# Optimization experiments

Measured on AMD Instinct MI355X. Metric: run time of the kernel, lower is better.

The kernel has to match this reference:

```python
import jax, jax.numpy as jnp
import numpy as np

B, T, D, H = 4, 4096, 1280, 5120  # batch, tokens (64x64 SAM grid), embedding_dim, mlp_dim


def setup_inputs() -> dict:
    key = jax.random.key(0)
    k = jax.random.split(key, 5)
    # int8 quantized activations and weights (symmetric, per-tensor)
    x = jax.random.randint(k[0], (B, T, D), -128, 128, dtype=jnp.int8)
    w1 = jax.random.randint(k[1], (H, D), -128, 128, dtype=jnp.int8)  # lin1.weight [out,in]
    b1 = jax.random.normal(k[2], (H,), jnp.float32) * 0.02            # fp32 bias
    w2 = jax.random.randint(k[3], (D, H), -128, 128, dtype=jnp.int8)  # lin2.weight [out,in]
    b2 = jax.random.normal(k[4], (D,), jnp.float32) * 0.02
    a1 = jnp.float32(0.05 * 0.01)   # input_scale * w1_scale (dequant alpha of lin1)
    s_req = jnp.float32(0.08)       # lin2_input_scale (requant scale after GELU)
    a2 = jnp.float32(0.08 * 0.01)   # lin2_input_scale * w2_scale (dequant alpha of lin2)
    return dict(x=x, w1=w1, b1=b1, w2=w2, b2=b2, a1=a1, s_req=s_req, a2=a2)


def reference(x, w1, b1, w2, b2, a1, s_req, a2):
    acc1 = jnp.einsum('btd,hd->bth', x.astype(jnp.int32), w1.astype(jnp.int32))
    h = acc1.astype(jnp.float32) * a1 + b1              # [B,T,H] fp32
    # exact (erf) GELU, then requantize to int8 for lin2's input
    g = jax.nn.gelu(h, approximate=False)
    q = jnp.clip(jnp.round(g / s_req), -128, 127).astype(jnp.int8)
    acc2 = jnp.einsum('bth,dh->btd', q.astype(jnp.int32), w2.astype(jnp.int32))
    return acc2.astype(jnp.float32) * a2 + b2           # [B,T,D] fp32
```

## Files before the change

kernel.cpp:

```cpp
#include <hip/hip_runtime.h>
#include <stdint.h>
#include <math.h>

typedef __attribute__((ext_vector_type(4))) int i32x4;
typedef __attribute__((ext_vector_type(16))) int i32x16;
typedef __attribute__((ext_vector_type(4))) float f32x4;

constexpr int D_DIM = 1280;
constexpr int H_DIM = 5120;

__device__ __forceinline__ void gload_lds16(const void* g, void* l) {
  __builtin_amdgcn_global_load_lds(
      (const __attribute__((address_space(1))) void*)g,
      (__attribute__((address_space(3))) void*)l,
      16, 0, 0);
}

__global__ void __launch_bounds__(256) k_packw(const int* __restrict__ s1,
                                               const int* __restrict__ s2,
                                               int8_t* __restrict__ out,
                                               long wn) {
  long i = ((long)blockIdx.x * 256 + threadIdx.x) * 16;
  const int* p = (i < wn) ? (s1 + i) : (s2 + (i - wn));
  i32x4 a = *(const i32x4*)(p);
  i32x4 b = *(const i32x4*)(p + 4);
  i32x4 c = *(const i32x4*)(p + 8);
  i32x4 d = *(const i32x4*)(p + 12);
  i32x4 r;
  r.x = (a.x & 255) | ((a.y & 255) << 8) | ((a.z & 255) << 16) | (a.w << 24);
  r.y = (b.x & 255) | ((b.y & 255) << 8) | ((b.z & 255) << 16) | (b.w << 24);
  r.z = (c.x & 255) | ((c.y & 255) << 8) | ((c.z & 255) << 16) | (c.w << 24);
  r.w = (d.x & 255) | ((d.y & 255) << 8) | ((d.z & 255) << 16) | (d.w << 24);
  *(i32x4*)(out + i) = r;
}

__global__ void __launch_bounds__(256) k_pack(const int* __restrict__ in,
                                              int8_t* __restrict__ out,
                                              long n) {
  long i = ((long)blockIdx.x * 256 + threadIdx.x) * 16;
  if (i >= n) return;
  const int* p = in + i;
  i32x4 a = *(const i32x4*)(p);
  i32x4 b = *(const i32x4*)(p + 4);
  i32x4 c = *(const i32x4*)(p + 8);
  i32x4 d = *(const i32x4*)(p + 12);
  i32x4 r;
  r.x = (a.x & 255) | ((a.y & 255) << 8) | ((a.z & 255) << 16) | (a.w << 24);
  r.y = (b.x & 255) | ((b.y & 255) << 8) | ((b.z & 255) << 16) | (b.w << 24);
  r.z = (c.x & 255) | ((c.y & 255) << 8) | ((c.z & 255) << 16) | (c.w << 24);
  r.w = (d.x & 255) | ((d.y & 255) << 8) | ((d.z & 255) << 16) | (d.w << 24);
  *(i32x4*)(out + i) = r;
}

template <int KDIM, int NDIM, bool GELU>
__global__ void __launch_bounds__(256, 2)
k_gemm(const int8_t* __restrict__ A, const int8_t* __restrict__ B,
       const float* __restrict__ bias, const float* __restrict__ ps1,
       const float* __restrict__ ps2, void* __restrict__ Cout, int Mtiles) {
  constexpr int BM = 128, BN = 128, BKB = 128;
  constexpr int NT = KDIM / BKB;
  constexpr int BNC = NDIM / BN;
  constexpr int G = BNC * 4;

  __shared__ __align__(16) int8_t smem[4 * 16384];

  const int nwg = Mtiles * BNC;
  int bm, bn;
  {
    const int bid = blockIdx.x;
    const int q = nwg >> 3, r = nwg & 7, x = bid & 7, l = bid >> 3;
    const int swz = (x < r ? x * (q + 1) : r * (q + 1) + (x - r) * q) + l;
    if ((Mtiles & 3) == 0) {
      const int g = swz / G, rr = swz % G;
      bn = rr >> 2;
      bm = g * 4 + (rr & 3);
    } else {
      bn = swz % BNC;
      bm = swz / BNC;
    }
  }

  const int tid = threadIdx.x;
  const int lane = tid & 63, wid = tid >> 6;
  const int wr = wid >> 1, wc = wid & 1;

  const int srow = tid >> 3;
  const int soff = (((tid & 7) ^ (srow & 7)) << 4);
  const int8_t* Ath = A + (size_t)(bm * BM + srow) * KDIM + soff;
  const int8_t* Bth = B + (size_t)(bn * BN + srow) * KDIM + soff;
  const int dT = tid * 16;

  auto STAGE = [&](int boff, const int8_t* ga, const int8_t* gb) {
#pragma unroll
    for (int p = 0; p < 4; ++p)
      gload_lds16(ga + (size_t)(p * 32) * KDIM, smem + boff + dT + p * 4096);
#pragma unroll
    for (int p = 0; p < 4; ++p)
      gload_lds16(gb + (size_t)(p * 32) * KDIM,
                  smem + 32768 + boff + dT + p * 4096);
  };

  const int r32 = lane & 31, hi5 = lane >> 5;
  const int fsw = (lane & 7) << 4;
  const int kq = hi5 << 4;
  const int8_t* aP[4];
  const int8_t* bP[4];
#pragma unroll
  for (int ks = 0; ks < 4; ++ks) {
    const int koff = (ks * 32 + kq) ^ fsw;
    aP[ks] = smem + (wr * 64 + r32) * BKB + koff;
    bP[ks] = smem + 32768 + (wc * 64 + r32) * BKB + koff;
  }

  i32x16 acc[2][2] = {};

  auto COMPUTE = [&](int boff) {
#pragma unroll
    for (int ks = 0; ks < 4; ++ks) {
      i32x4 a0 = *(const i32x4*)(aP[ks] + boff);
      i32x4 a1 = *(const i32x4*)(aP[ks] + boff + 4096);
      i32x4 b0 = *(const i32x4*)(bP[ks] + boff);
      i32x4 b1 = *(const i32x4*)(bP[ks] + boff + 4096);
      if constexpr (GELU) {
        acc[0][0] = __builtin_amdgcn_mfma_i32_32x32x32_i8(b0, a0, acc[0][0], 0, 0, 0);
        acc[0][1] = __builtin_amdgcn_mfma_i32_32x32x32_i8(b0, a1, acc[0][1], 0, 0, 0);
        acc[1][0] = __builtin_amdgcn_mfma_i32_32x32x32_i8(b1, a0, acc[1][0], 0, 0, 0);
        acc[1][1] = __builtin_amdgcn_mfma_i32_32x32x32_i8(b1, a1, acc[1][1], 0, 0, 0);
      } else {
        acc[0][0] = __builtin_amdgcn_mfma_i32_32x32x32_i8(a0, b0, acc[0][0], 0, 0, 0);
        acc[0][1] = __builtin_amdgcn_mfma_i32_32x32x32_i8(a0, b1, acc[0][1], 0, 0, 0);
        acc[1][0] = __builtin_amdgcn_mfma_i32_32x32x32_i8(a1, b0, acc[1][0], 0, 0, 0);
        acc[1][1] = __builtin_amdgcn_mfma_i32_32x32x32_i8(a1, b1, acc[1][1], 0, 0, 0);
      }
    }
  };

  STAGE(0, Ath, Bth);
  __syncthreads();
  const int8_t* gA = Ath + BKB;
  const int8_t* gB = Bth + BKB;
#pragma unroll 1
  for (int t = 0; t < NT; t += 2) {
    STAGE(16384, gA, gB);
    COMPUTE(0);
    __syncthreads();
    if (t + 2 < NT) STAGE(0, gA + BKB, gB + BKB);
    COMPUTE(16384);
    __syncthreads();
    gA += 2 * BKB;
    gB += 2 * BKB;
  }

  if constexpr (GELU) {
    const float s1 = *ps1;
    const float rs = 1.0f / (*ps2);
    int8_t* Q = (int8_t*)Cout;
    int8_t* lb = smem;
#pragma unroll
    for (int n = 0; n < 2; ++n) {
#pragma unroll
      for (int q = 0; q < 4; ++q) {
        const int hl = wc * 64 + n * 32 + q * 8 + hi5 * 4;
        const f32x4 bv = *(const f32x4*)(bias + bn * BN + hl);
#pragma unroll
        for (int m = 0; m < 2; ++m) {
          const int tok = wr * 64 + m * 32 + r32;
          uint32_t pk = 0;
#pragma unroll
          for (int rr = 0; rr < 4; ++rr) {
            const float h = __builtin_fmaf((float)acc[n][m][q * 4 + rr], s1, bv[rr]);
            const float e = __expf(-1.702f * h);
            const float g = h * __builtin_amdgcn_rcpf(1.0f + e);
            float qf = rintf(g * rs);
            qf = fminf(127.0f, fmaxf(-128.0f, qf));
            pk |= ((uint32_t)((int)qf & 255)) << (rr * 8);
          }
          *(uint32_t*)(lb + tok * 132 + hl) = pk;
        }
      }
    }
    __syncthreads();
#pragma unroll
    for (int it = 0; it < 4; ++it) {
      const int row = it * 32 + (tid >> 3);
      const int sl = tid & 7;
      const int8_t* rp = lb + row * 132 + sl * 16;
      i32x4 v;
      v.x = *(const int*)(rp);
      v.y = *(const int*)(rp + 4);
      v.z = *(const int*)(rp + 8);
      v.w = *(const int*)(rp + 12);
      *(i32x4*)(Q + (size_t)(bm * BM + row) * NDIM + bn * BN + sl * 16) = v;
    }
  } else {
    const float s1 = *ps1;
    float* O = (float*)Cout;
    const int colb = bn * BN + wc * 64 + r32;
#pragma unroll
    for (int n = 0; n < 2; ++n) {
      const int col = colb + n * 32;
      const float bv = bias[col];
#pragma unroll
      for (int m = 0; m < 2; ++m) {
        const int rowb = bm * BM + wr * 64 + m * 32 + hi5 * 4;
#pragma unroll
        for (int q = 0; q < 4; ++q)
#pragma unroll
          for (int rr = 0; rr < 4; ++rr) {
            const int row = rowb + q * 8 + rr;
            O[(size_t)row * NDIM + col] =
                __builtin_fmaf((float)acc[m][n][q * 4 + rr], s1, bv);
          }
      }
    }
  }
}

extern "C" void kernel_launch(void* const* d_in, const int* in_sizes, int n_in,
                              void* d_out, int out_size, void* d_ws, size_t ws_size,
                              hipStream_t stream) {
  (void)in_sizes; (void)n_in; (void)out_size;
  const int*   x32  = (const int*)d_in[0];
  const int*   w132 = (const int*)d_in[1];
  const float* b1   = (const float*)d_in[2];
  const int*   w232 = (const int*)d_in[3];
  const float* b2   = (const float*)d_in[4];
  const float* a1   = (const float*)d_in[5];
  const float* sreq = (const float*)d_in[6];
  const float* a2   = (const float*)d_in[7];
  float* out = (float*)d_out;

  const int M = 4 * 4096;
  const size_t WN = (size_t)H_DIM * D_DIM;
  constexpr int BM = 128, BN = 128;

  int8_t* w1p  = (int8_t*)d_ws;
  int8_t* w2p  = w1p + WN;
  int8_t* base = w2p + WN;

  size_t avail = ws_size > 2 * WN ? ws_size - 2 * WN : 0;
  size_t rows = avail / (size_t)(D_DIM + H_DIM);
  int Mc = (int)((rows / BM) * BM);
  if (Mc > M) Mc = M;
  if (Mc < BM) Mc = BM;

  k_packw<<<(int)(2 * WN / 4096), 256, 0, stream>>>(w132, w232, w1p, (long)WN);

  for (int m0 = 0; m0 < M; m0 += Mc) {
    const int mc = (M - m0 < Mc) ? (M - m0) : Mc;
    int8_t* xp = base;
    int8_t* q  = base + (size_t)Mc * D_DIM;
    const size_t nx = (size_t)mc * D_DIM;
    const int mt = mc / BM;
    k_pack<<<(int)(nx / 4096), 256, 0, stream>>>(x32 + (size_t)m0 * D_DIM, xp, (long)nx);
    k_gemm<D_DIM, H_DIM, true><<<mt * (H_DIM / BN), 256, 0, stream>>>(
        xp, w1p, b1, a1, sreq, q, mt);
    k_gemm<H_DIM, D_DIM, false><<<mt * (D_DIM / BN), 256, 0, stream>>>(
        q, w2p, b2, a2, nullptr, out + (size_t)m0 * D_DIM, mt);
  }
}
```

Baseline: 284.4 us.

## Triple-buffer A tiles with asynchronous vmcnt waits and MFMA priority hints

Reworks the GEMM main loop from a two-stage double buffer with full __syncthreads into a pipeline: the A tile uses three LDS slots, B uses two, and loads are issued one or two iterations ahead. Explicit s_waitcnt vmcnt plus a raw s_barrier replace the per-half syncthreads, and s_setprio raises wave priority around the MFMA bursts. The goal is to hide global-to-LDS latency and reduce barrier stalls. LDS use grows from 64KB to 80KB per block, which may limit two blocks per CU, and the hand-set vmcnt counts must match the number of loads in flight.

```diff
diff --git a/kernel.cpp b/kernel.cpp
--- a/kernel.cpp
+++ b/kernel.cpp
@@ -61,8 +61,9 @@
   constexpr int NT = KDIM / BKB;
   constexpr int BNC = NDIM / BN;
   constexpr int G = BNC * 4;
-
-  __shared__ __align__(16) int8_t smem[4 * 16384];
+  constexpr int BOFF = 49152;
+
+  __shared__ __align__(16) int8_t smem[81920];
 
   const int nwg = Mtiles * BNC;
   int bm, bn;
@@ -90,37 +91,41 @@
   const int8_t* Bth = B + (size_t)(bn * BN + srow) * KDIM + soff;
   const int dT = tid * 16;
 
-  auto STAGE = [&](int boff, const int8_t* ga, const int8_t* gb) {
+  auto STAGE_A = [&](int slot, int tt) {
+    const int8_t* g = Ath + tt * BKB;
 #pragma unroll
     for (int p = 0; p < 4; ++p)
-      gload_lds16(ga + (size_t)(p * 32) * KDIM, smem + boff + dT + p * 4096);
+      gload_lds16(g + (size_t)(p * 32) * KDIM, smem + slot * 16384 + dT + p * 4096);
+  };
+  auto STAGE_B = [&](int slot, int tt) {
+    const int8_t* g = Bth + tt * BKB;
 #pragma unroll
     for (int p = 0; p < 4; ++p)
-      gload_lds16(gb + (size_t)(p * 32) * KDIM,
-                  smem + 32768 + boff + dT + p * 4096);
+      gload_lds16(g + (size_t)(p * 32) * KDIM,
+                  smem + BOFF + slot * 16384 + dT + p * 4096);
   };
 
   const int r32 = lane & 31, hi5 = lane >> 5;
   const int fsw = (lane & 7) << 4;
   const int kq = hi5 << 4;
-  const int8_t* aP[4];
-  const int8_t* bP[4];
-#pragma unroll
-  for (int ks = 0; ks < 4; ++ks) {
-    const int koff = (ks * 32 + kq) ^ fsw;
-    aP[ks] = smem + (wr * 64 + r32) * BKB + koff;
-    bP[ks] = smem + 32768 + (wc * 64 + r32) * BKB + koff;
-  }
+  int koff[4];
+#pragma unroll
+  for (int ks = 0; ks < 4; ++ks) koff[ks] = ((ks * 32 + kq) ^ fsw);
+  const int rowA = (wr * 64 + r32) * BKB;
+  const int rowB = (wc * 64 + r32) * BKB;
 
   i32x16 acc[2][2] = {};
 
-  auto COMPUTE = [&](int boff) {
+  auto COMPUTE = [&](int aoff, int boff) {
+    const int8_t* Ab = smem + aoff + rowA;
+    const int8_t* Bb = smem + BOFF + boff + rowB;
 #pragma unroll
     for (int ks = 0; ks < 4; ++ks) {
-      i32x4 a0 = *(const i32x4*)(aP[ks] + boff);
-      i32x4 a1 = *(const i32x4*)(aP[ks] + boff + 4096);
-      i32x4 b0 = *(const i32x4*)(bP[ks] + boff);
-      i32x4 b1 = *(const i32x4*)(bP[ks] + boff + 4096);
+      i32x4 a0 = *(const i32x4*)(Ab + koff[ks]);
+      i32x4 a1 = *(const i32x4*)(Ab + 4096 + koff[ks]);
+      i32x4 b0 = *(const i32x4*)(Bb + koff[ks]);
+      i32x4 b1 = *(const i32x4*)(Bb + 4096 + koff[ks]);
+      __builtin_amdgcn_s_setprio(1);
       if constexpr (GELU) {
         acc[0][0] = __builtin_amdgcn_mfma_i32_32x32x32_i8(b0, a0, acc[0][0], 0, 0, 0);
         acc[0][1] = __builtin_amdgcn_mfma_i32_32x32x32_i8(b0, a1, acc[0][1], 0, 0, 0);
@@ -132,26 +137,33 @@
         acc[1][0] = __builtin_amdgcn_mfma_i32_32x32x32_i8(a1, b0, acc[1][0], 0, 0, 0);
         acc[1][1] = __builtin_amdgcn_mfma_i32_32x32x32_i8(a1, b1, acc[1][1], 0, 0, 0);
       }
+      __builtin_amdgcn_s_setprio(0);
     }
   };
 
-  STAGE(0, Ath, Bth);
-  __syncthreads();
-  const int8_t* gA = Ath + BKB;
-  const int8_t* gB = Bth + BKB;
+  STAGE_B(0, 0);
+  STAGE_A(0, 0);
+  STAGE_A(1, 1);
+
+  int acur = 0;
+  int astg = 2;
 #pragma unroll 1
-  for (int t = 0; t < NT; t += 2) {
-    STAGE(16384, gA, gB);
-    COMPUTE(0);
+  for (int t = 0; t < NT; ++t) {
+    if (t + 1 < NT)
+      asm volatile("s_waitcnt vmcnt(4)" ::: "memory");
+    else
+      asm volatile("s_waitcnt vmcnt(0)" ::: "memory");
+    __builtin_amdgcn_s_barrier();
+    __builtin_amdgcn_sched_barrier(0);
+    if (t + 1 < NT) STAGE_B((t + 1) & 1, t + 1);
+    if (t + 2 < NT) STAGE_A(astg, t + 2);
+    COMPUTE(acur * 16384, (t & 1) * 16384);
+    acur = acur == 2 ? 0 : acur + 1;
+    astg = astg == 2 ? 0 : astg + 1;
+  }
+
+  if constexpr (GELU) {
     __syncthreads();
-    if (t + 2 < NT) STAGE(0, gA + BKB, gB + BKB);
-    COMPUTE(16384);
-    __syncthreads();
-    gA += 2 * BKB;
-    gB += 2 * BKB;
-  }
-
-  if constexpr (GELU) {
     const float s1 = *ps1;
     const float rs = 1.0f / (*ps2);
     int8_t* Q = (int8_t*)Cout;
```

Result: slower. 302.3 us (+6.3%).

## Load weight fragments directly into registers instead of staging through LDS

Applied to the files above, without the earlier changes.

The weight operand is no longer copied into shared memory. Each wave reads its MFMA weight fragments straight from global memory into registers, double-buffered one K-step ahead, so shared memory holds only the activation tile (32 KB instead of 64 KB). This removes half of the LDS traffic and LDS reads per step, and raises MFMA issue priority with s_setprio around each MFMA group. In exchange, the two waves sharing a column block each fetch the same weights, the global reads are strided per row rather than staged cooperatively, and register pressure goes up.

```diff
diff --git a/kernel.cpp b/kernel.cpp
--- a/kernel.cpp
+++ b/kernel.cpp
@@ -54,7 +54,7 @@
 
 template <int KDIM, int NDIM, bool GELU>
 __global__ void __launch_bounds__(256, 2)
-k_gemm(const int8_t* __restrict__ A, const int8_t* __restrict__ B,
+k_gemm(const int8_t* __restrict__ A, const int8_t* __restrict__ W,
        const float* __restrict__ bias, const float* __restrict__ ps1,
        const float* __restrict__ ps2, void* __restrict__ Cout, int Mtiles) {
   constexpr int BM = 128, BN = 128, BKB = 128;
@@ -62,7 +62,7 @@
   constexpr int BNC = NDIM / BN;
   constexpr int G = BNC * 4;
 
-  __shared__ __align__(16) int8_t smem[4 * 16384];
+  __shared__ __align__(16) int8_t smem[32768];
 
   const int nwg = Mtiles * BNC;
   int bm, bn;
@@ -83,72 +83,75 @@
   const int tid = threadIdx.x;
   const int lane = tid & 63, wid = tid >> 6;
   const int wr = wid >> 1, wc = wid & 1;
+  const int r32 = lane & 31, hi5 = lane >> 5;
 
   const int srow = tid >> 3;
   const int soff = (((tid & 7) ^ (srow & 7)) << 4);
   const int8_t* Ath = A + (size_t)(bm * BM + srow) * KDIM + soff;
-  const int8_t* Bth = B + (size_t)(bn * BN + srow) * KDIM + soff;
   const int dT = tid * 16;
 
-  auto STAGE = [&](int boff, const int8_t* ga, const int8_t* gb) {
+  auto STAGE = [&](int boff, int tt) {
+    const int8_t* g = Ath + tt * BKB;
 #pragma unroll
     for (int p = 0; p < 4; ++p)
-      gload_lds16(ga + (size_t)(p * 32) * KDIM, smem + boff + dT + p * 4096);
-#pragma unroll
-    for (int p = 0; p < 4; ++p)
-      gload_lds16(gb + (size_t)(p * 32) * KDIM,
-                  smem + 32768 + boff + dT + p * 4096);
+      gload_lds16(g + (size_t)(p * 32) * KDIM, smem + boff + dT + p * 4096);
   };
 
-  const int r32 = lane & 31, hi5 = lane >> 5;
+  const int8_t* W0 = W + (size_t)(bn * BN + wc * 64 + r32) * KDIM + (hi5 << 4);
+  const int8_t* W1p = W0 + (size_t)32 * KDIM;
+  i32x4 wfA[8], wfB[8];
+  auto LOADW = [&](i32x4 (&wf)[8], int tt) {
+    const int o = tt * BKB;
+#pragma unroll
+    for (int ks = 0; ks < 4; ++ks) {
+      wf[2 * ks]     = *(const i32x4*)(W0 + o + ks * 32);
+      wf[2 * ks + 1] = *(const i32x4*)(W1p + o + ks * 32);
+    }
+  };
+
   const int fsw = (lane & 7) << 4;
   const int kq = hi5 << 4;
-  const int8_t* aP[4];
-  const int8_t* bP[4];
-#pragma unroll
-  for (int ks = 0; ks < 4; ++ks) {
-    const int koff = (ks * 32 + kq) ^ fsw;
-    aP[ks] = smem + (wr * 64 + r32) * BKB + koff;
-    bP[ks] = smem + 32768 + (wc * 64 + r32) * BKB + koff;
-  }
+  int koff[4];
+#pragma unroll
+  for (int ks = 0; ks < 4; ++ks) koff[ks] = ((ks * 32 + kq) ^ fsw);
+  const int rowA = (wr * 64 + r32) * BKB;
 
   i32x16 acc[2][2] = {};
 
-  auto COMPUTE = [&](int boff) {
+  auto COMPUTE = [&](int boff, const i32x4 (&wf)[8]) {
+    const int8_t* Ab = smem + boff + rowA;
 #pragma unroll
     for (int ks = 0; ks < 4; ++ks) {
-      i32x4 a0 = *(const i32x4*)(aP[ks] + boff);
-      i32x4 a1 = *(const i32x4*)(aP[ks] + boff + 4096);
-      i32x4 b0 = *(const i32x4*)(bP[ks] + boff);
-      i32x4 b1 = *(const i32x4*)(bP[ks] + boff + 4096);
+      i32x4 a0 = *(const i32x4*)(Ab + koff[ks]);
+      i32x4 a1 = *(const i32x4*)(Ab + 4096 + koff[ks]);
+      __builtin_amdgcn_s_setprio(1);
       if constexpr (GELU) {
-        acc[0][0] = __builtin_amdgcn_mfma_i32_32x32x32_i8(b0, a0, acc[0][0], 0, 0, 0);
-        acc[0][1] = __builtin_amdgcn_mfma_i32_32x32x32_i8(b0, a1, acc[0][1], 0, 0, 0);
-        acc[1][0] = __builtin_amdgcn_mfma_i32_32x32x32_i8(b1, a0, acc[1][0], 0, 0, 0);
-        acc[1][1] = __builtin_amdgcn_mfma_i32_32x32x32_i8(b1, a1, acc[1][1], 0, 0, 0);
+        acc[0][0] = __builtin_amdgcn_mfma_i32_32x32x32_i8(wf[2*ks],   a0, acc[0][0], 0, 0, 0);
+        acc[0][1] = __builtin_amdgcn_mfma_i32_32x32x32_i8(wf[2*ks],   a1, acc[0][1], 0, 0, 0);
+        acc[1][0] = __builtin_amdgcn_mfma_i32_32x32x32_i8(wf[2*ks+1], a0, acc[1][0], 0, 0, 0);
+        acc[1][1] = __builtin_amdgcn_mfma_i32_32x32x32_i8(wf[2*ks+1], a1, acc[1][1], 0, 0, 0);
       } else {
-        acc[0][0] = __builtin_amdgcn_mfma_i32_32x32x32_i8(a0, b0, acc[0][0], 0, 0, 0);
-        acc[0][1] = __builtin_amdgcn_mfma_i32_32x32x32_i8(a0, b1, acc[0][1], 0, 0, 0);
-        acc[1][0] = __builtin_amdgcn_mfma_i32_32x32x32_i8(a1, b0, acc[1][0], 0, 0, 0);
-        acc[1][1] = __builtin_amdgcn_mfma_i32_32x32x32_i8(a1, b1, acc[1][1], 0, 0, 0);
+        acc[0][0] = __builtin_amdgcn_mfma_i32_32x32x32_i8(a0, wf[2*ks],   acc[0][0], 0, 0, 0);
+        acc[0][1] = __builtin_amdgcn_mfma_i32_32x32x32_i8(a0, wf[2*ks+1], acc[0][1], 0, 0, 0);
+        acc[1][0] = __builtin_amdgcn_mfma_i32_32x32x32_i8(a1, wf[2*ks],   acc[1][0], 0, 0, 0);
+        acc[1][1] = __builtin_amdgcn_mfma_i32_32x32x32_i8(a1, wf[2*ks+1], acc[1][1], 0, 0, 0);
       }
+      __builtin_amdgcn_s_setprio(0);
     }
   };
 
-  STAGE(0, Ath, Bth);
+  STAGE(0, 0);
+  LOADW(wfA, 0);
   __syncthreads();
-  const int8_t* gA = Ath + BKB;
-  const int8_t* gB = Bth + BKB;
 #pragma unroll 1
   for (int t = 0; t < NT; t += 2) {
-    STAGE(16384, gA, gB);
-    COMPUTE(0);
+    STAGE(16384, t + 1);
+    LOADW(wfB, t + 1);
+    COMPUTE(0, wfA);
     __syncthreads();
-    if (t + 2 < NT) STAGE(0, gA + BKB, gB + BKB);
-    COMPUTE(16384);
+    if (t + 2 < NT) { STAGE(0, t + 2); LOADW(wfA, t + 2); }
+    COMPUTE(16384, wfB);
     __syncthreads();
-    gA += 2 * BKB;
-    gB += 2 * BKB;
   }
 
   if constexpr (GELU) {
```

After: 491.5 us. 1.73x slower.
